# Optimization experiments

Measured on AMD Instinct MI355X. Metric: run time of the kernel, lower is better.

The kernel has to match this reference:

```python
import jax, jax.numpy as jnp
import numpy as np

B, N, T = 1, 4096, 512
WQ, HK = 32, 128
ATOM_S, ATOM_Z, TOKEN_S, TOKEN_Z = 128, 16, 384, 128
FEAT = 3 + 1 + 128 + 4 * 64  # 388


def _indexing_matrix(K, Wq, Hk):
    # faithful port of get_indexing_matrix: one-hot banded gather matrix [2K, K*h]
    h = Hk // (Wq // 2)
    ar = jnp.arange(2 * K)
    idx = jnp.clip(ar[None, :] - ar[:, None] + h // 2, 0, h + 1)
    idx = idx.reshape(K, 2, 2 * K)[:, 0, :]                 # [K, 2K]
    oh = jax.nn.one_hot(idx, h + 2, dtype=jnp.float32)[..., 1:-1]  # [K, 2K, h]
    return jnp.transpose(oh, (1, 0, 2)).reshape(2 * K, K * h)


def _to_keys(x, M, Wq, Hk):
    b, n, d = x.shape
    k = n // Wq
    x = x.reshape(b, 2 * k, Wq // 2, d)
    return jnp.einsum('bjid,jk->bkid', x, M).reshape(b, k, Hk, d)


def _ln(x, g, b, eps=1e-5):
    m = jnp.mean(x, axis=-1, keepdims=True)
    v = jnp.var(x, axis=-1, keepdims=True)
    return (x - m) * jax.lax.rsqrt(v + eps) * g + b


def setup_inputs() -> dict:
    key = jax.random.key(0)
    ks = jax.random.split(key, 24)
    s = 0.02
    tok_idx = jnp.sort(jax.random.randint(ks[0], (B, N), 0, T), axis=-1)
    return {
        'ref_pos': jax.random.normal(ks[1], (B, N, 3), jnp.float32),
        'ref_charge': jax.random.normal(ks[2], (B, N), jnp.float32),
        'ref_element': jax.random.uniform(ks[3], (B, N, 128), jnp.float32),
        'ref_atom_name_chars': jax.random.uniform(ks[4], (B, N, 4, 64), jnp.float32),
        'atom_pad_mask': jnp.ones((B, N), dtype=bool),
        'ref_space_uid': jnp.sort(jax.random.randint(ks[5], (B, N), 0, 512), axis=-1),
        'atom_to_token': jax.nn.one_hot(tok_idx, T, dtype=jnp.float32),
        's_trunk': jax.random.normal(ks[6], (B, T, TOKEN_S), jnp.float32),
        'z': jax.random.normal(ks[7], (B, T, T, TOKEN_Z), jnp.float32),
        # learned params, stored [in, out] so y = x @ W (+ b)
        'W_feat': jax.random.normal(ks[8], (FEAT, ATOM_S), jnp.float32) * s,
        'b_feat': jnp.zeros((ATOM_S,), jnp.float32),
        'W_pos': jax.random.normal(ks[9], (3, ATOM_Z), jnp.float32) * s,
        'W_dist': jax.random.normal(ks[10], (1, ATOM_Z), jnp.float32) * s,
        'W_mask': jax.random.normal(ks[11], (1, ATOM_Z), jnp.float32) * s,
        'ln_s_g': jnp.ones((TOKEN_S,), jnp.float32),
        'ln_s_b': jnp.zeros((TOKEN_S,), jnp.float32),
        'W_s2c': jax.random.normal(ks[12], (TOKEN_S, ATOM_S), jnp.float32) * s,
        'ln_z_g': jnp.ones((TOKEN_Z,), jnp.float32),
        'ln_z_b': jnp.zeros((TOKEN_Z,), jnp.float32),
        'W_z2p': jax.random.normal(ks[13], (TOKEN_Z, ATOM_Z), jnp.float32) * s,
        'W_cq': jax.random.normal(ks[14], (ATOM_S, ATOM_Z), jnp.float32) * s,
        'W_ck': jax.random.normal(ks[15], (ATOM_S, ATOM_Z), jnp.float32) * s,
        'W_m1': jax.random.normal(ks[16], (ATOM_Z, ATOM_Z), jnp.float32) * s,
        'W_m2': jax.random.normal(ks[17], (ATOM_Z, ATOM_Z), jnp.float32) * s,
        'W_m3': jax.random.normal(ks[18], (ATOM_Z, ATOM_Z), jnp.float32) * s,
    }


def reference(ref_pos, ref_charge, ref_element, ref_atom_name_chars, atom_pad_mask,
              ref_space_uid, atom_to_token, s_trunk, z,
              W_feat, b_feat, W_pos, W_dist, W_mask,
              ln_s_g, ln_s_b, W_s2c, ln_z_g, ln_z_b, W_z2p,
              W_cq, W_ck, W_m1, W_m2, W_m3):
    b, n, _ = ref_pos.shape
    k = n // WQ
    atom_feats = jnp.concatenate(
        [ref_pos, ref_charge[..., None], ref_element,
         ref_atom_name_chars.reshape(b, n, 4 * 64)], axis=-1)
    c = atom_feats @ W_feat + b_feat                       # [B,N,atom_s]
    q = c
    M = _indexing_matrix(k, WQ, HK)
    tk = lambda x: _to_keys(x, M, WQ, HK)

    pos_q = ref_pos.reshape(b, k, WQ, 1, 3)
    pos_k = tk(ref_pos).reshape(b, k, 1, HK, 3)
    d = pos_k - pos_q                                      # [B,K,W,H,3]
    d_norm = 1.0 / (1.0 + jnp.sum(d * d, axis=-1, keepdims=True))

    mq = atom_pad_mask.reshape(b, k, WQ, 1)
    mk = tk(atom_pad_mask[..., None].astype(jnp.float32)).reshape(b, k, 1, HK) > 0.5
    uq = ref_space_uid.reshape(b, k, WQ, 1)
    uk = tk(ref_space_uid[..., None].astype(jnp.float32)).reshape(b, k, 1, HK).astype(ref_space_uid.dtype)
    v = (mq & mk & (uq == uk)).astype(jnp.float32)[..., None]  # [B,K,W,H,1]

    p = (d @ W_pos) * v
    p = p + (d_norm @ W_dist) * v
    p = p + (v @ W_mask) * v

    # structure_prediction branch
    s2c = _ln(s_trunk, ln_s_g, ln_s_b) @ W_s2c             # [B,T,atom_s]
    c = c + jnp.einsum('bnt,btd->bnd', atom_to_token, s2c)
    a2t_q = atom_to_token.reshape(b, k, WQ, -1)            # [B,K,W,T]
    a2t_k = tk(atom_to_token)                              # [B,K,H,T]
    zp = _ln(z, ln_z_g, ln_z_b) @ W_z2p                    # [B,T,T,atom_z]
    tmp = jnp.einsum('bwki,bijd->bwkjd', a2t_q, zp)        # [B,K,W,T,atom_z]
    p = p + jnp.einsum('bwkjd,bwlj->bwkld', tmp, a2t_k)    # [B,K,W,H,atom_z]

    p = p + jax.nn.relu(c).reshape(b, k, WQ, 1, -1) @ W_cq
    p = p + jax.nn.relu(tk(c)).reshape(b, k, 1, HK, -1) @ W_ck

    h1 = jax.nn.relu(p) @ W_m1
    h2 = jax.nn.relu(h1) @ W_m2
    p = p + jax.nn.relu(h2) @ W_m3
    return (q, c, p)
```

## Files before the change

### kernel.cpp

```cpp
#include <hip/hip_runtime.h>

#define N_ATOMS 4096
#define T_TOK   512
#define TOKEN_S 384
#define TOKEN_Z 128

using bfrag = __attribute__((ext_vector_type(8))) short;
using f4    = __attribute__((ext_vector_type(4))) float;

__device__ __forceinline__ short f2bf(float f) {
    unsigned u = __float_as_uint(f);
    unsigned r = u + 0x7FFFu + ((u >> 16) & 1u);
    return (short)(r >> 16);
}
__device__ __forceinline__ float bf2f(short s) {
    return __uint_as_float(((unsigned)(unsigned short)s) << 16);
}

__global__ __launch_bounds__(256) void tok_kernel(const float* __restrict__ a2t,
                                                  int* __restrict__ tok) {
    const int wave = threadIdx.x >> 6, lane = threadIdx.x & 63;
    const int n = blockIdx.x * 4 + wave;
    if (n >= N_ATOMS) return;
    const float* row = a2t + (size_t)n * T_TOK;
    int found = 0;
#pragma unroll
    for (int m = 0; m < T_TOK / 64; ++m)
        if (row[lane + 64 * m] > 0.5f) found = lane + 64 * m;
#pragma unroll
    for (int off = 32; off >= 1; off >>= 1)
        found = max(found, __shfl_xor(found, off, 64));
    if (lane == 0) tok[n] = found;
}

__global__ __launch_bounds__(256) void prep_kernel(
    const float* __restrict__ Wz, const float* __restrict__ gz,
    const float* __restrict__ bz, const float* __restrict__ Wf,
    const float* __restrict__ Wcq, const float* __restrict__ Wck,
    short* __restrict__ zpW, short* __restrict__ featW,
    short* __restrict__ WcqF, short* __restrict__ WckF,
    float* __restrict__ bias16, float* __restrict__ cs16) {
    if (blockIdx.x == 27) {
        const int t = threadIdx.x;
        if (t < 16) {
            float s = 0.f;
            for (int k = 0; k < 128; ++k) s += bz[k] * Wz[k * 16 + t];
            bias16[t] = s;
        } else if (t < 32) {
            const int n = t - 16;
            float s = 0.f;
            for (int k = 0; k < 128; ++k) s += gz[k] * Wz[k * 16 + n];
            cs16[n] = s;
        }
        return;
    }
    const int id = blockIdx.x * 256 + threadIdx.x;
    const int lane = id & 63, fs = id >> 6;
    const int quad = lane >> 4, n = lane & 15;
    short v[8];
    short* dst;
    if (fs < 4) {
#pragma unroll
        for (int j = 0; j < 8; ++j) {
            int k = fs * 32 + quad * 8 + j;
            v[j] = f2bf(gz[k] * Wz[k * 16 + n]);
        }
        dst = zpW + (size_t)(fs * 64 + lane) * 8;
    } else if (fs < 100) {
        const int idx = fs - 4, kb = idx >> 3, nt = idx & 7;
#pragma unroll
        for (int j = 0; j < 8; ++j) {
            int f = 4 + kb * 32 + quad * 8 + j;
            v[j] = f2bf(Wf[(size_t)f * 128 + nt * 16 + n]);
        }
        dst = featW + (size_t)(idx * 64 + lane) * 8;
    } else if (fs < 104) {
        const int kb = fs - 100;
#pragma unroll
        for (int j = 0; j < 8; ++j) {
            int k = kb * 32 + quad * 8 + j;
            v[j] = f2bf(Wcq[k * 16 + n]);
        }
        dst = WcqF + (size_t)(kb * 64 + lane) * 8;
    } else {
        const int kb = fs - 104;
#pragma unroll
        for (int j = 0; j < 8; ++j) {
            int k = kb * 32 + quad * 8 + j;
            v[j] = f2bf(Wck[k * 16 + n]);
        }
        dst = WckF + (size_t)(kb * 64 + lane) * 8;
    }
#pragma unroll
    for (int j = 0; j < 8; ++j) dst[j] = v[j];
}

__global__ __launch_bounds__(128) void s2c_kernel(
    const float* __restrict__ s_trunk, const float* __restrict__ g,
    const float* __restrict__ bb, const float* __restrict__ W,
    float* __restrict__ s2c) {
    __shared__ float xln[8 * TOKEN_S];
    const int wv = threadIdx.x >> 6, lane = threadIdx.x & 63;
    const int t0 = blockIdx.x * 8;
    for (int tt = wv; tt < 8; tt += 2) {
        const float* row = s_trunk + (size_t)(t0 + tt) * TOKEN_S;
        float vals[6];
        float s = 0.f, sq = 0.f;
#pragma unroll
        for (int m = 0; m < 6; ++m) {
            float v = row[lane + 64 * m];
            vals[m] = v; s += v; sq += v * v;
        }
#pragma unroll
        for (int off = 32; off >= 1; off >>= 1) {
            s += __shfl_xor(s, off, 64);
            sq += __shfl_xor(sq, off, 64);
        }
        float mean = s * (1.f / TOKEN_S);
        float var = sq * (1.f / TOKEN_S) - mean * mean;
        float rstd = rsqrtf(var + 1e-5f);
#pragma unroll
        for (int m = 0; m < 6; ++m) {
            int f = lane + 64 * m;
            xln[tt * TOKEN_S + f] = (vals[m] - mean) * rstd * g[f] + bb[f];
        }
    }
    __syncthreads();
    const int d = threadIdx.x;
    float acc[8];
#pragma unroll
    for (int tt = 0; tt < 8; ++tt) acc[tt] = 0.f;
    for (int f = 0; f < TOKEN_S; ++f) {
        float w = W[(size_t)f * 128 + d];
#pragma unroll
        for (int tt = 0; tt < 8; ++tt) acc[tt] += xln[tt * TOKEN_S + f] * w;
    }
#pragma unroll
    for (int tt = 0; tt < 8; ++tt)
        s2c[(size_t)(t0 + tt) * 128 + d] = acc[tt];
}

__global__ __launch_bounds__(256) void zp_mfma_kernel(
    const float* __restrict__ z, const short* __restrict__ zpW,
    const float* __restrict__ bias16, const float* __restrict__ cs16,
    float* __restrict__ zp) {
    __shared__ short zt[4][16 * 136];
    const int wave = threadIdx.x >> 6, lane = threadIdx.x & 63;
    const int m = lane & 15, quad = lane >> 4;
    const size_t tile = (size_t)blockIdx.x * 4 + wave;
    const size_t r0 = tile * 16;
    const float* zb = z + r0 * 128;
    short* tw = &zt[wave][0];
#pragma unroll
    for (int i = 0; i < 8; ++i) {
        const int flat = i * 256 + lane * 4;
        float4 v = *(const float4*)(zb + flat);
        const int r = flat >> 7, c = flat & 127;
        int2 pk;
        pk.x = ((unsigned)(unsigned short)f2bf(v.y) << 16) |
               (unsigned)(unsigned short)f2bf(v.x);
        pk.y = ((unsigned)(unsigned short)f2bf(v.w) << 16) |
               (unsigned)(unsigned short)f2bf(v.z);
        *(int2*)&tw[r * 136 + c] = pk;
    }
    __syncthreads();
    bfrag A[4];
    float xs = 0.f, xq = 0.f;
#pragma unroll
    for (int kb = 0; kb < 4; ++kb) {
        A[kb] = *(const bfrag*)&tw[m * 136 + kb * 32 + quad * 8];
#pragma unroll
        for (int j = 0; j < 8; ++j) {
            float xv = bf2f(A[kb][j]);
            xs += xv; xq = fmaf(xv, xv, xq);
        }
    }
    xs += __shfl_xor(xs, 16, 64); xs += __shfl_xor(xs, 32, 64);
    xq += __shfl_xor(xq, 16, 64); xq += __shfl_xor(xq, 32, 64);
    const float mean = xs * (1.f / 128.f);
    const float var  = xq * (1.f / 128.f) - mean * mean;
    const float rstd = rsqrtf(var + 1e-5f);
    const float mrs  = mean * rstd;

    const bfrag* wb = (const bfrag*)zpW;
    f4 acc = {0.f, 0.f, 0.f, 0.f};
#pragma unroll
    for (int kb = 0; kb < 4; ++kb)
        acc = __builtin_amdgcn_mfma_f32_16x16x32_bf16(A[kb], wb[kb * 64 + lane],
                                                      acc, 0, 0, 0);
    const float csn = cs16[m], bn = bias16[m];
    float* orow = zp + r0 * 16;
#pragma unroll
    for (int reg = 0; reg < 4; ++reg) {
        const int r = quad * 4 + reg;
        float rs = __shfl(rstd, r, 64);
        float ms = __shfl(mrs, r, 64);
        orow[r * 16 + m] = rs * acc[reg] - ms * csn + bn;
    }
}

__global__ __launch_bounds__(64) void featcatk_kernel(
    const float* __restrict__ pos, const float* __restrict__ charge,
    const float* __restrict__ elem, const float* __restrict__ namec,
    const float* __restrict__ Wf, const float* __restrict__ bf,
    const float* __restrict__ s2c, const int* __restrict__ tok,
    const short* __restrict__ featW, const short* __restrict__ WcqF,
    const short* __restrict__ WckF, float* __restrict__ q_out,
    float* __restrict__ c_out, float* __restrict__ acq,
    float* __restrict__ ack) {
    __shared__ short ctile[16 * 136];
    const int lane = threadIdx.x;
    const int m = lane & 15, quad = lane >> 4;
    const int a0 = blockIdx.x * 16;

    f4 acc[8];
#pragma unroll
    for (int nt = 0; nt < 8; ++nt) acc[nt] = (f4){0.f, 0.f, 0.f, 0.f};
    const bfrag* Bb = (const bfrag*)featW;
#pragma unroll
    for (int kb = 0; kb < 12; ++kb) {
        const int f0 = kb * 32 + quad * 8;
        const float* src = (kb < 4)
            ? (elem + (size_t)(a0 + m) * 128 + f0)
            : (namec + (size_t)(a0 + m) * 256 + f0 - 128);
        float4 x0 = ((const float4*)src)[0];
        float4 x1 = ((const float4*)src)[1];
        bfrag A;
        A[0] = f2bf(x0.x); A[1] = f2bf(x0.y); A[2] = f2bf(x0.z); A[3] = f2bf(x0.w);
        A[4] = f2bf(x1.x); A[5] = f2bf(x1.y); A[6] = f2bf(x1.z); A[7] = f2bf(x1.w);
#pragma unroll
        for (int nt = 0; nt < 8; ++nt)
            acc[nt] = __builtin_amdgcn_mfma_f32_16x16x32_bf16(
                A, Bb[(kb * 8 + nt) * 64 + lane], acc[nt], 0, 0, 0);
    }
    float px[4], py[4], pz[4], ch[4];
    int tk4[4];
#pragma unroll
    for (int reg = 0; reg < 4; ++reg) {
        const int a = a0 + quad * 4 + reg;
        px[reg] = pos[a * 3 + 0]; py[reg] = pos[a * 3 + 1];
        pz[reg] = pos[a * 3 + 2]; ch[reg] = charge[a];
        tk4[reg] = tok[a];
    }
#pragma unroll
    for (int nt = 0; nt < 8; ++nt) {
        const int cn = nt * 16 + m;
        const float w0 = Wf[cn], w1 = Wf[128 + cn], w2 = Wf[256 + cn],
                    w3 = Wf[384 + cn], bv = bf[cn];
#pragma unroll
        for (int reg = 0; reg < 4; ++reg) {
            const int r = quad * 4 + reg;
            float qv = acc[nt][reg] + px[reg] * w0 + py[reg] * w1 +
                       pz[reg] * w2 + ch[reg] * w3 + bv;
            q_out[(size_t)(a0 + r) * 128 + cn] = qv;
            float cv = qv + s2c[(size_t)tk4[reg] * 128 + cn];
            c_out[(size_t)(a0 + r) * 128 + cn] = cv;
            ctile[r * 136 + cn] = f2bf(fmaxf(cv, 0.f));
        }
    }
    __syncthreads();
    f4 a2[2] = {{0.f, 0.f, 0.f, 0.f}, {0.f, 0.f, 0.f, 0.f}};
    const bfrag* Bq = (const bfrag*)WcqF;
    const bfrag* Bk = (const bfrag*)WckF;
#pragma unroll
    for (int kb = 0; kb < 4; ++kb) {
        bfrag Af = *(const bfrag*)&ctile[m * 136 + kb * 32 + quad * 8];
        a2[0] = __builtin_amdgcn_mfma_f32_16x16x32_bf16(Af, Bq[kb * 64 + lane],
                                                        a2[0], 0, 0, 0);
        a2[1] = __builtin_amdgcn_mfma_f32_16x16x32_bf16(Af, Bk[kb * 64 + lane],
                                                        a2[1], 0, 0, 0);
    }
#pragma unroll
    for (int reg = 0; reg < 4; ++reg) {
        const int r = quad * 4 + reg;
        acq[(size_t)(a0 + r) * 16 + m] = a2[0][reg];
        ack[(size_t)(a0 + r) * 16 + m] = a2[1][reg];
    }
}

__global__ __launch_bounds__(256) void pair_mfma_kernel(
    const float* __restrict__ pos, const int* __restrict__ uid,
    const int* __restrict__ tok, const float* __restrict__ zp,
    const float* __restrict__ acq, const float* __restrict__ ack,
    const float* __restrict__ W_pos, const float* __restrict__ W_dist,
    const float* __restrict__ W_mask, const float* __restrict__ W_m1,
    const float* __restrict__ W_m2, const float* __restrict__ W_m3,
    float* __restrict__ p_out) {
    const int wave = threadIdx.x >> 6, lane = threadIdx.x & 63;
    const int m = lane & 15, quad = lane >> 4;
    const int qa = blockIdx.x * 4 + wave;
    const int j = qa >> 5;

    bfrag A1, A2, A3;
#pragma unroll
    for (int jj = 0; jj < 4; ++jj) {
        const int d = quad * 4 + jj;
        A1[jj] = f2bf(W_m1[d * 16 + m]); A1[jj + 4] = 0;
        A2[jj] = f2bf(W_m2[d * 16 + m]); A2[jj + 4] = 0;
        A3[jj] = f2bf(W_m3[d * 16 + m]); A3[jj + 4] = 0;
    }
    float wp0[4], wp1[4], wp2[4], wd[4], wm[4];
#pragma unroll
    for (int jj = 0; jj < 4; ++jj) {
        const int d = quad * 4 + jj;
        wp0[jj] = W_pos[d]; wp1[jj] = W_pos[16 + d]; wp2[jj] = W_pos[32 + d];
        wd[jj] = W_dist[d]; wm[jj] = W_mask[d];
    }
    const float pqx = pos[qa * 3 + 0], pqy = pos[qa * 3 + 1],
                pqz = pos[qa * 3 + 2];
    const int uq = uid[qa], tq = tok[qa];
    const float4 aq = *(const float4*)(acq + (size_t)qa * 16 + quad * 4);
    const float aqv[4] = {aq.x, aq.y, aq.z, aq.w};
    float* pbase = p_out + (size_t)qa * 2048;

    const f4 zero = {0.f, 0.f, 0.f, 0.f};
#pragma unroll
    for (int g = 0; g < 8; ++g) {
        const int kk = g * 16 + m;
        const int src = j * 32 + kk - 48;
        const bool valid = ((unsigned)src < (unsigned)N_ATOMS);
        float dx = 0.f, dy = 0.f, dz = 0.f, dn = 0.f, vflag = 0.f;
        float zv[4] = {0.f, 0.f, 0.f, 0.f}, av[4] = {0.f, 0.f, 0.f, 0.f};
        if (valid) {
            dx = pos[src * 3 + 0] - pqx;
            dy = pos[src * 3 + 1] - pqy;
            dz = pos[src * 3 + 2] - pqz;
            dn = 1.f / (1.f + dx * dx + dy * dy + dz * dz);
            vflag = (uid[src] == uq) ? 1.f : 0.f;
            const int tk_ = tok[src];
            float4 zl = *(const float4*)(zp + ((size_t)tq * 512 + tk_) * 16 + quad * 4);
            float4 al = *(const float4*)(ack + (size_t)src * 16 + quad * 4);
            zv[0] = zl.x; zv[1] = zl.y; zv[2] = zl.z; zv[3] = zl.w;
            av[0] = al.x; av[1] = al.y; av[2] = al.z; av[3] = al.w;
        }
        float pb[4];
        bfrag B;
#pragma unroll
        for (int jj = 0; jj < 4; ++jj) {
            float t = dx * wp0[jj] + dy * wp1[jj] + dz * wp2[jj] +
                      dn * wd[jj] + wm[jj];
            pb[jj] = vflag * t + zv[jj] + av[jj] + aqv[jj];
            B[jj] = f2bf(fmaxf(pb[jj], 0.f));
            B[jj + 4] = 0;
        }
        f4 t1 = __builtin_amdgcn_mfma_f32_16x16x32_bf16(A1, B, zero, 0, 0, 0);
        bfrag B2;
#pragma unroll
        for (int jj = 0; jj < 4; ++jj) {
            B2[jj] = f2bf(fmaxf(t1[jj], 0.f)); B2[jj + 4] = 0;
        }
        f4 t2 = __builtin_amdgcn_mfma_f32_16x16x32_bf16(A2, B2, zero, 0, 0, 0);
        bfrag B3;
#pragma unroll
        for (int jj = 0; jj < 4; ++jj) {
            B3[jj] = f2bf(fmaxf(t2[jj], 0.f)); B3[jj + 4] = 0;
        }
        f4 t3 = __builtin_amdgcn_mfma_f32_16x16x32_bf16(A3, B3, zero, 0, 0, 0);
        float4 o = make_float4(pb[0] + t3[0], pb[1] + t3[1],
                               pb[2] + t3[2], pb[3] + t3[3]);
        *(float4*)(pbase + kk * 16 + quad * 4) = o;
    }
}

extern "C" void kernel_launch(void* const* d_in, const int* in_sizes, int n_in,
                              void* d_out, int out_size, void* d_ws, size_t ws_size,
                              hipStream_t stream) {
    const float* ref_pos     = (const float*)d_in[0];
    const float* ref_charge  = (const float*)d_in[1];
    const float* ref_element = (const float*)d_in[2];
    const float* ref_name    = (const float*)d_in[3];
    const int*   uid         = (const int*)d_in[5];
    const float* a2t         = (const float*)d_in[6];
    const float* s_trunk     = (const float*)d_in[7];
    const float* z           = (const float*)d_in[8];
    const float* W_feat      = (const float*)d_in[9];
    const float* b_feat      = (const float*)d_in[10];
    const float* W_pos       = (const float*)d_in[11];
    const float* W_dist      = (const float*)d_in[12];
    const float* W_mask      = (const float*)d_in[13];
    const float* ln_s_g      = (const float*)d_in[14];
    const float* ln_s_b      = (const float*)d_in[15];
    const float* W_s2c       = (const float*)d_in[16];
    const float* ln_z_g      = (const float*)d_in[17];
    const float* ln_z_b      = (const float*)d_in[18];
    const float* W_z2p       = (const float*)d_in[19];
    const float* W_cq        = (const float*)d_in[20];
    const float* W_ck        = (const float*)d_in[21];
    const float* W_m1        = (const float*)d_in[22];
    const float* W_m2        = (const float*)d_in[23];
    const float* W_m3        = (const float*)d_in[24];

    float* out = (float*)d_out;
    float* q_out = out;
    float* c_out = out + 524288;
    float* p_out = out + 1048576;

    float* zp   = (float*)d_ws;
    float* s2c  = zp + 4194304;
    float* acq  = s2c + 65536;
    float* ack  = acq + 65536;
    int*   tok  = (int*)(ack + 65536);
    short* zpW   = (short*)(tok + 4096);
    short* featW = zpW + 2048;
    short* WcqF  = featW + 49152;
    short* WckF  = WcqF + 2048;
    float* bias16 = (float*)(WckF + 2048);
    float* cs16   = bias16 + 16;

    tok_kernel<<<1024, 256, 0, stream>>>(a2t, tok);
    prep_kernel<<<28, 256, 0, stream>>>(W_z2p, ln_z_g, ln_z_b, W_feat,
                                        W_cq, W_ck, zpW, featW, WcqF, WckF,
                                        bias16, cs16);
    s2c_kernel<<<64, 128, 0, stream>>>(s_trunk, ln_s_g, ln_s_b, W_s2c, s2c);
    zp_mfma_kernel<<<4096, 256, 0, stream>>>(z, zpW, bias16, cs16, zp);
    featcatk_kernel<<<256, 64, 0, stream>>>(ref_pos, ref_charge, ref_element,
                                            ref_name, W_feat, b_feat, s2c, tok,
                                            featW, WcqF, WckF,
                                            q_out, c_out, acq, ack);
    pair_mfma_kernel<<<1024, 256, 0, stream>>>(ref_pos, uid, tok, zp, acq, ack,
                                               W_pos, W_dist, W_mask,
                                               W_m1, W_m2, W_m3, p_out);
}
```

Before: 327.4 us.

## Merge setup kernels, MFMA s2c, bf16 zp intermediate, split featcatk waves

Combines the token-lookup and weight-prep kernels into one setup launch, and replaces the scalar s2c LayerNorm+matmul with an MFMA kernel that folds the LayerNorm affine into precomputed weights. zp_mfma now reads z directly into registers instead of staging through LDS, and stores the zp intermediate as bf16 to halve its write and gather traffic. featcatk is split across two waves to add parallelism. The cost is extra bf16 rounding of zp and of the s2c inputs.

```diff
diff --git a/kernel.cpp b/kernel.cpp
--- a/kernel.cpp
+++ b/kernel.cpp
@@ -13,48 +13,61 @@
     unsigned r = u + 0x7FFFu + ((u >> 16) & 1u);
     return (short)(r >> 16);
 }
-__device__ __forceinline__ float bf2f(short s) {
-    return __uint_as_float(((unsigned)(unsigned short)s) << 16);
-}
-
-__global__ __launch_bounds__(256) void tok_kernel(const float* __restrict__ a2t,
-                                                  int* __restrict__ tok) {
-    const int wave = threadIdx.x >> 6, lane = threadIdx.x & 63;
-    const int n = blockIdx.x * 4 + wave;
-    if (n >= N_ATOMS) return;
-    const float* row = a2t + (size_t)n * T_TOK;
-    int found = 0;
-#pragma unroll
-    for (int m = 0; m < T_TOK / 64; ++m)
-        if (row[lane + 64 * m] > 0.5f) found = lane + 64 * m;
-#pragma unroll
-    for (int off = 32; off >= 1; off >>= 1)
-        found = max(found, __shfl_xor(found, off, 64));
-    if (lane == 0) tok[n] = found;
-}
-
-__global__ __launch_bounds__(256) void prep_kernel(
-    const float* __restrict__ Wz, const float* __restrict__ gz,
-    const float* __restrict__ bz, const float* __restrict__ Wf,
-    const float* __restrict__ Wcq, const float* __restrict__ Wck,
-    short* __restrict__ zpW, short* __restrict__ featW,
-    short* __restrict__ WcqF, short* __restrict__ WckF,
-    float* __restrict__ bias16, float* __restrict__ cs16) {
-    if (blockIdx.x == 27) {
-        const int t = threadIdx.x;
-        if (t < 16) {
-            float s = 0.f;
-            for (int k = 0; k < 128; ++k) s += bz[k] * Wz[k * 16 + t];
-            bias16[t] = s;
-        } else if (t < 32) {
-            const int n = t - 16;
-            float s = 0.f;
-            for (int k = 0; k < 128; ++k) s += gz[k] * Wz[k * 16 + n];
-            cs16[n] = s;
-        }
+__device__ __forceinline__ float bf2f(unsigned short s) {
+    return __uint_as_float(((unsigned)s) << 16);
+}
+
+__global__ __launch_bounds__(256) void setup_kernel(
+    const float* __restrict__ a2t, const float* __restrict__ Wz,
+    const float* __restrict__ gz, const float* __restrict__ bz,
+    const float* __restrict__ Wf, const float* __restrict__ Wcq,
+    const float* __restrict__ Wck, const float* __restrict__ Ws2c,
+    const float* __restrict__ gs, const float* __restrict__ bs,
+    int* __restrict__ tok, short* __restrict__ zpW,
+    short* __restrict__ featW, short* __restrict__ WcqF,
+    short* __restrict__ WckF, short* __restrict__ s2cW,
+    float* __restrict__ bias16, float* __restrict__ cs16,
+    float* __restrict__ cs128, float* __restrict__ bs128) {
+    const int b = blockIdx.x, tid = threadIdx.x;
+    if (b >= 53) {
+        const int wave = tid >> 6, lane = tid & 63;
+        const int n = (b - 53) * 4 + wave;
+        const float* row = a2t + (size_t)n * T_TOK;
+        int found = 0;
+#pragma unroll
+        for (int m = 0; m < T_TOK / 64; ++m)
+            if (row[lane + 64 * m] > 0.5f) found = lane + 64 * m;
+#pragma unroll
+        for (int off = 32; off >= 1; off >>= 1)
+            found = max(found, __shfl_xor(found, off, 64));
+        if (lane == 0) tok[n] = found;
         return;
     }
-    const int id = blockIdx.x * 256 + threadIdx.x;
+    if (b == 51) {
+        const int o = tid >> 3, s = tid & 7;
+        const float* vec = (o < 16) ? bz : gz;
+        const int n = o & 15;
+        float p = 0.f;
+#pragma unroll
+        for (int i = 0; i < 16; ++i) {
+            const int k = s + 8 * i;
+            p += vec[k] * Wz[k * 16 + n];
+        }
+        p += __shfl_xor(p, 1, 64); p += __shfl_xor(p, 2, 64);
+        p += __shfl_xor(p, 4, 64);
+        if (s == 0) { if (o < 16) bias16[n] = p; else cs16[n] = p; }
+        return;
+    }
+    if (b == 52) {
+        const int o = tid & 127, arr = tid >> 7;
+        const float* vec = arr ? bs : gs;
+        float s = 0.f;
+        for (int k = 0; k < TOKEN_S; ++k)
+            s += vec[k] * Ws2c[(size_t)k * 128 + o];
+        if (arr) bs128[o] = s; else cs128[o] = s;
+        return;
+    }
+    const int id = b * 256 + tid;
     const int lane = id & 63, fs = id >> 6;
     const int quad = lane >> 4, n = lane & 15;
     short v[8];
@@ -82,7 +95,7 @@
             v[j] = f2bf(Wcq[k * 16 + n]);
         }
         dst = WcqF + (size_t)(kb * 64 + lane) * 8;
-    } else {
+    } else if (fs < 108) {
         const int kb = fs - 104;
 #pragma unroll
         for (int j = 0; j < 8; ++j) {
@@ -90,95 +103,94 @@
             v[j] = f2bf(Wck[k * 16 + n]);
         }
         dst = WckF + (size_t)(kb * 64 + lane) * 8;
+    } else {
+        const int idx = fs - 108, kb = idx >> 3, nt = idx & 7;
+#pragma unroll
+        for (int j = 0; j < 8; ++j) {
+            int k = kb * 32 + quad * 8 + j;
+            v[j] = f2bf(gs[k] * Ws2c[(size_t)k * 128 + nt * 16 + n]);
+        }
+        dst = s2cW + (size_t)(idx * 64 + lane) * 8;
     }
 #pragma unroll
     for (int j = 0; j < 8; ++j) dst[j] = v[j];
 }
 
-__global__ __launch_bounds__(128) void s2c_kernel(
-    const float* __restrict__ s_trunk, const float* __restrict__ g,
-    const float* __restrict__ bb, const float* __restrict__ W,
+__global__ __launch_bounds__(256) void s2c_mfma_kernel(
+    const float* __restrict__ s_trunk, const short* __restrict__ s2cW,
+    const float* __restrict__ cs128, const float* __restrict__ bs128,
     float* __restrict__ s2c) {
-    __shared__ float xln[8 * TOKEN_S];
-    const int wv = threadIdx.x >> 6, lane = threadIdx.x & 63;
-    const int t0 = blockIdx.x * 8;
-    for (int tt = wv; tt < 8; tt += 2) {
-        const float* row = s_trunk + (size_t)(t0 + tt) * TOKEN_S;
-        float vals[6];
-        float s = 0.f, sq = 0.f;
-#pragma unroll
-        for (int m = 0; m < 6; ++m) {
-            float v = row[lane + 64 * m];
-            vals[m] = v; s += v; sq += v * v;
-        }
-#pragma unroll
-        for (int off = 32; off >= 1; off >>= 1) {
-            s += __shfl_xor(s, off, 64);
-            sq += __shfl_xor(sq, off, 64);
-        }
-        float mean = s * (1.f / TOKEN_S);
-        float var = sq * (1.f / TOKEN_S) - mean * mean;
-        float rstd = rsqrtf(var + 1e-5f);
-#pragma unroll
-        for (int m = 0; m < 6; ++m) {
-            int f = lane + 64 * m;
-            xln[tt * TOKEN_S + f] = (vals[m] - mean) * rstd * g[f] + bb[f];
-        }
-    }
-    __syncthreads();
-    const int d = threadIdx.x;
-    float acc[8];
-#pragma unroll
-    for (int tt = 0; tt < 8; ++tt) acc[tt] = 0.f;
-    for (int f = 0; f < TOKEN_S; ++f) {
-        float w = W[(size_t)f * 128 + d];
-#pragma unroll
-        for (int tt = 0; tt < 8; ++tt) acc[tt] += xln[tt * TOKEN_S + f] * w;
-    }
-#pragma unroll
-    for (int tt = 0; tt < 8; ++tt)
-        s2c[(size_t)(t0 + tt) * 128 + d] = acc[tt];
+    const int wave = threadIdx.x >> 6, lane = threadIdx.x & 63;
+    const int m = lane & 15, quad = lane >> 4;
+    const int wg = blockIdx.x * 4 + wave;
+    const int tile = wg >> 3, nt = wg & 7;
+    const int t0 = tile * 16;
+    const float* xrow = s_trunk + (size_t)(t0 + m) * TOKEN_S;
+
+    bfrag A[12];
+    float xs = 0.f, xq = 0.f;
+#pragma unroll
+    for (int kb = 0; kb < 12; ++kb) {
+        const float4* p = (const float4*)(xrow + kb * 32 + quad * 8);
+        float4 x0 = p[0], x1 = p[1];
+        const float xv[8] = {x0.x, x0.y, x0.z, x0.w, x1.x, x1.y, x1.z, x1.w};
+#pragma unroll
+        for (int j = 0; j < 8; ++j) {
+            A[kb][j] = f2bf(xv[j]);
+            xs += xv[j]; xq = fmaf(xv[j], xv[j], xq);
+        }
+    }
+    xs += __shfl_xor(xs, 16, 64); xs += __shfl_xor(xs, 32, 64);
+    xq += __shfl_xor(xq, 16, 64); xq += __shfl_xor(xq, 32, 64);
+    const float mean = xs * (1.f / TOKEN_S);
+    const float var  = xq * (1.f / TOKEN_S) - mean * mean;
+    const float rstd = rsqrtf(var + 1e-5f);
+    const float mrs  = mean * rstd;
+
+    const bfrag* Bb = (const bfrag*)s2cW;
+    f4 acc = {0.f, 0.f, 0.f, 0.f};
+#pragma unroll
+    for (int kb = 0; kb < 12; ++kb)
+        acc = __builtin_amdgcn_mfma_f32_16x16x32_bf16(
+            A[kb], Bb[(kb * 8 + nt) * 64 + lane], acc, 0, 0, 0);
+
+    const int cn = nt * 16 + m;
+    const float csn = cs128[cn], bsn = bs128[cn];
+#pragma unroll
+    for (int reg = 0; reg < 4; ++reg) {
+        const int r = quad * 4 + reg;
+        const float rs = __shfl(rstd, r, 64);
+        const float ms = __shfl(mrs, r, 64);
+        s2c[(size_t)(t0 + r) * 128 + cn] = rs * acc[reg] - ms * csn + bsn;
+    }
 }
 
 __global__ __launch_bounds__(256) void zp_mfma_kernel(
     const float* __restrict__ z, const short* __restrict__ zpW,
     const float* __restrict__ bias16, const float* __restrict__ cs16,
-    float* __restrict__ zp) {
-    __shared__ short zt[4][16 * 136];
+    unsigned short* __restrict__ zp_bf) {
     const int wave = threadIdx.x >> 6, lane = threadIdx.x & 63;
     const int m = lane & 15, quad = lane >> 4;
-    const size_t tile = (size_t)blockIdx.x * 4 + wave;
-    const size_t r0 = tile * 16;
-    const float* zb = z + r0 * 128;
-    short* tw = &zt[wave][0];
-#pragma unroll
-    for (int i = 0; i < 8; ++i) {
-        const int flat = i * 256 + lane * 4;
-        float4 v = *(const float4*)(zb + flat);
-        const int r = flat >> 7, c = flat & 127;
-        int2 pk;
-        pk.x = ((unsigned)(unsigned short)f2bf(v.y) << 16) |
-               (unsigned)(unsigned short)f2bf(v.x);
-        pk.y = ((unsigned)(unsigned short)f2bf(v.w) << 16) |
-               (unsigned)(unsigned short)f2bf(v.z);
-        *(int2*)&tw[r * 136 + c] = pk;
-    }
-    __syncthreads();
+    const size_t r0 = ((size_t)blockIdx.x * 4 + wave) * 16;
+    const float* zrow = z + (r0 + m) * (size_t)TOKEN_Z;
+
     bfrag A[4];
     float xs = 0.f, xq = 0.f;
 #pragma unroll
     for (int kb = 0; kb < 4; ++kb) {
-        A[kb] = *(const bfrag*)&tw[m * 136 + kb * 32 + quad * 8];
-#pragma unroll
-        for (int j = 0; j < 8; ++j) {
-            float xv = bf2f(A[kb][j]);
-            xs += xv; xq = fmaf(xv, xv, xq);
+        const float4* p = (const float4*)(zrow + kb * 32 + quad * 8);
+        float4 x0 = p[0], x1 = p[1];
+        const float xv[8] = {x0.x, x0.y, x0.z, x0.w, x1.x, x1.y, x1.z, x1.w};
+#pragma unroll
+        for (int j = 0; j < 8; ++j) {
+            A[kb][j] = f2bf(xv[j]);
+            xs += xv[j]; xq = fmaf(xv[j], xv[j], xq);
         }
     }
     xs += __shfl_xor(xs, 16, 64); xs += __shfl_xor(xs, 32, 64);
     xq += __shfl_xor(xq, 16, 64); xq += __shfl_xor(xq, 32, 64);
-    const float mean = xs * (1.f / 128.f);
-    const float var  = xq * (1.f / 128.f) - mean * mean;
+    const float mean = xs * (1.f / TOKEN_Z);
+    const float var  = xq * (1.f / TOKEN_Z) - mean * mean;
     const float rstd = rsqrtf(var + 1e-5f);
     const float mrs  = mean * rstd;
 
@@ -189,17 +201,17 @@
         acc = __builtin_amdgcn_mfma_f32_16x16x32_bf16(A[kb], wb[kb * 64 + lane],
                                                       acc, 0, 0, 0);
     const float csn = cs16[m], bn = bias16[m];
-    float* orow = zp + r0 * 16;
 #pragma unroll
     for (int reg = 0; reg < 4; ++reg) {
         const int r = quad * 4 + reg;
-        float rs = __shfl(rstd, r, 64);
-        float ms = __shfl(mrs, r, 64);
-        orow[r * 16 + m] = rs * acc[reg] - ms * csn + bn;
-    }
-}
-
-__global__ __launch_bounds__(64) void featcatk_kernel(
+        const float rs = __shfl(rstd, r, 64);
+        const float ms = __shfl(mrs, r, 64);
+        zp_bf[(r0 + r) * 16 + m] =
+            (unsigned short)f2bf(rs * acc[reg] - ms * csn + bn);
+    }
+}
+
+__global__ __launch_bounds__(128) void featcatk_kernel(
     const float* __restrict__ pos, const float* __restrict__ charge,
     const float* __restrict__ elem, const float* __restrict__ namec,
     const float* __restrict__ Wf, const float* __restrict__ bf,
@@ -209,13 +221,14 @@
     float* __restrict__ c_out, float* __restrict__ acq,
     float* __restrict__ ack) {
     __shared__ short ctile[16 * 136];
-    const int lane = threadIdx.x;
+    const int wave = threadIdx.x >> 6, lane = threadIdx.x & 63;
     const int m = lane & 15, quad = lane >> 4;
     const int a0 = blockIdx.x * 16;
-
-    f4 acc[8];
-#pragma unroll
-    for (int nt = 0; nt < 8; ++nt) acc[nt] = (f4){0.f, 0.f, 0.f, 0.f};
+    const int ntb = wave * 4;
+
+    f4 acc[4];
+#pragma unroll
+    for (int nt = 0; nt < 4; ++nt) acc[nt] = (f4){0.f, 0.f, 0.f, 0.f};
     const bfrag* Bb = (const bfrag*)featW;
 #pragma unroll
     for (int kb = 0; kb < 12; ++kb) {
@@ -229,9 +242,9 @@
         A[0] = f2bf(x0.x); A[1] = f2bf(x0.y); A[2] = f2bf(x0.z); A[3] = f2bf(x0.w);
         A[4] = f2bf(x1.x); A[5] = f2bf(x1.y); A[6] = f2bf(x1.z); A[7] = f2bf(x1.w);
 #pragma unroll
-        for (int nt = 0; nt < 8; ++nt)
+        for (int nt = 0; nt < 4; ++nt)
             acc[nt] = __builtin_amdgcn_mfma_f32_16x16x32_bf16(
-                A, Bb[(kb * 8 + nt) * 64 + lane], acc[nt], 0, 0, 0);
+                A, Bb[(kb * 8 + ntb + nt) * 64 + lane], acc[nt], 0, 0, 0);
     }
     float px[4], py[4], pz[4], ch[4];
     int tk4[4];
@@ -243,8 +256,8 @@
         tk4[reg] = tok[a];
     }
 #pragma unroll
-    for (int nt = 0; nt < 8; ++nt) {
-        const int cn = nt * 16 + m;
+    for (int nt = 0; nt < 4; ++nt) {
+        const int cn = (ntb + nt) * 16 + m;
         const float w0 = Wf[cn], w1 = Wf[128 + cn], w2 = Wf[256 + cn],
                     w3 = Wf[384 + cn], bv = bf[cn];
 #pragma unroll
@@ -259,28 +272,23 @@
         }
     }
     __syncthreads();
-    f4 a2[2] = {{0.f, 0.f, 0.f, 0.f}, {0.f, 0.f, 0.f, 0.f}};
-    const bfrag* Bq = (const bfrag*)WcqF;
-    const bfrag* Bk = (const bfrag*)WckF;
+    const bfrag* BW = wave ? (const bfrag*)WckF : (const bfrag*)WcqF;
+    float* dst = wave ? ack : acq;
+    f4 a2 = {0.f, 0.f, 0.f, 0.f};
 #pragma unroll
     for (int kb = 0; kb < 4; ++kb) {
         bfrag Af = *(const bfrag*)&ctile[m * 136 + kb * 32 + quad * 8];
-        a2[0] = __builtin_amdgcn_mfma_f32_16x16x32_bf16(Af, Bq[kb * 64 + lane],
-                                                        a2[0], 0, 0, 0);
-        a2[1] = __builtin_amdgcn_mfma_f32_16x16x32_bf16(Af, Bk[kb * 64 + lane],
-                                                        a2[1], 0, 0, 0);
-    }
-#pragma unroll
-    for (int reg = 0; reg < 4; ++reg) {
-        const int r = quad * 4 + reg;
-        acq[(size_t)(a0 + r) * 16 + m] = a2[0][reg];
-        ack[(size_t)(a0 + r) * 16 + m] = a2[1][reg];
-    }
+        a2 = __builtin_amdgcn_mfma_f32_16x16x32_bf16(Af, BW[kb * 64 + lane],
+                                                     a2, 0, 0, 0);
+    }
+#pragma unroll
+    for (int reg = 0; reg < 4; ++reg)
+        dst[(size_t)(a0 + quad * 4 + reg) * 16 + m] = a2[reg];
 }
 
 __global__ __launch_bounds__(256) void pair_mfma_kernel(
     const float* __restrict__ pos, const int* __restrict__ uid,
-    const int* __restrict__ tok, const float* __restrict__ zp,
+    const int* __restrict__ tok, const unsigned short* __restrict__ zp_bf,
     const float* __restrict__ acq, const float* __restrict__ ack,
     const float* __restrict__ W_pos, const float* __restrict__ W_dist,
     const float* __restrict__ W_mask, const float* __restrict__ W_m1,
@@ -328,9 +336,11 @@
             dn = 1.f / (1.f + dx * dx + dy * dy + dz * dz);
             vflag = (uid[src] == uq) ? 1.f : 0.f;
             const int tk_ = tok[src];
-            float4 zl = *(const float4*)(zp + ((size_t)tq * 512 + tk_) * 16 + quad * 4);
+            ushort4 zl = *(const ushort4*)(zp_bf +
+                            ((size_t)tq * 512 + tk_) * 16 + quad * 4);
             float4 al = *(const float4*)(ack + (size_t)src * 16 + quad * 4);
-            zv[0] = zl.x; zv[1] = zl.y; zv[2] = zl.z; zv[3] = zl.w;
+            zv[0] = bf2f(zl.x); zv[1] = bf2f(zl.y);
+            zv[2] = bf2f(zl.z); zv[3] = bf2f(zl.w);
             av[0] = al.x; av[1] = al.y; av[2] = al.z; av[3] = al.w;
         }
         float pb[4];
@@ -395,8 +405,9 @@
     float* c_out = out + 524288;
     float* p_out = out + 1048576;
 
-    float* zp   = (float*)d_ws;
-    float* s2c  = zp + 4194304;
+    char* w = (char*)d_ws;
+    unsigned short* zp_bf = (unsigned short*)w;
+    float* s2c  = (float*)(w + 8388608);
     float* acq  = s2c + 65536;
     float* ack  = acq + 65536;
     int*   tok  = (int*)(ack + 65536);
@@ -404,20 +415,24 @@
     short* featW = zpW + 2048;
     short* WcqF  = featW + 49152;
     short* WckF  = WcqF + 2048;
-    float* bias16 = (float*)(WckF + 2048);
+    short* s2cW  = WckF + 2048;
+    float* bias16 = (float*)(s2cW + 49152);
     float* cs16   = bias16 + 16;
-
-    tok_kernel<<<1024, 256, 0, stream>>>(a2t, tok);
-    prep_kernel<<<28, 256, 0, stream>>>(W_z2p, ln_z_g, ln_z_b, W_feat,
-                                        W_cq, W_ck, zpW, featW, WcqF, WckF,
-                                        bias16, cs16);
-    s2c_kernel<<<64, 128, 0, stream>>>(s_trunk, ln_s_g, ln_s_b, W_s2c, s2c);
-    zp_mfma_kernel<<<4096, 256, 0, stream>>>(z, zpW, bias16, cs16, zp);
-    featcatk_kernel<<<256, 64, 0, stream>>>(ref_pos, ref_charge, ref_element,
-                                            ref_name, W_feat, b_feat, s2c, tok,
-                                            featW, WcqF, WckF,
-                                            q_out, c_out, acq, ack);
-    pair_mfma_kernel<<<1024, 256, 0, stream>>>(ref_pos, uid, tok, zp, acq, ack,
-                                               W_pos, W_dist, W_mask,
+    float* cs128  = cs16 + 16;
+    float* bs128  = cs128 + 128;
+
+    setup_kernel<<<1077, 256, 0, stream>>>(a2t, W_z2p, ln_z_g, ln_z_b,
+                                           W_feat, W_cq, W_ck, W_s2c,
+                                           ln_s_g, ln_s_b, tok, zpW, featW,
+                                           WcqF, WckF, s2cW, bias16, cs16,
+                                           cs128, bs128);
+    s2c_mfma_kernel<<<64, 256, 0, stream>>>(s_trunk, s2cW, cs128, bs128, s2c);
+    zp_mfma_kernel<<<4096, 256, 0, stream>>>(z, zpW, bias16, cs16, zp_bf);
+    featcatk_kernel<<<256, 128, 0, stream>>>(ref_pos, ref_charge, ref_element,
+                                             ref_name, W_feat, b_feat, s2c, tok,
+                                             featW, WcqF, WckF,
+                                             q_out, c_out, acq, ack);
+    pair_mfma_kernel<<<1024, 256, 0, stream>>>(ref_pos, uid, tok, zp_bf,
+                                               acq, ack, W_pos, W_dist, W_mask,
                                                W_m1, W_m2, W_m3, p_out);
 }
```

Result: faster. 293.3 us (-10.4%).
